# Optimization experiments

Measured on AMD Instinct MI355X. Metric: run time of the kernel, lower is better.

## Reference

```python
import jax, jax.numpy as jnp
import numpy as np

N_NODES = 50000
N_EDGES = 800000
D = 256


def gcn_conv(x, edge_index, W, b, n_nodes):
    """PyG-style GCNConv: add self-loops, symmetric norm, linear, scatter-add."""
    # add self loops
    loops = jnp.arange(n_nodes, dtype=edge_index.dtype)
    src = jnp.concatenate([edge_index[0], loops])  # message sources
    dst = jnp.concatenate([edge_index[1], loops])  # aggregation targets
    # symmetric normalization: deg computed on targets (incl. self loops)
    deg = jax.ops.segment_sum(jnp.ones_like(dst, dtype=x.dtype), dst,
                              num_segments=n_nodes)
    dinv = jnp.where(deg > 0, jax.lax.rsqrt(deg), 0.0)
    norm = dinv[src] * dinv[dst]  # [E+N]
    h = x @ W  # [N, out]
    msg = h[src] * norm[:, None]  # gather + scale, [E+N, out]
    out = jax.ops.segment_sum(msg, dst, num_segments=n_nodes)  # scatter-add
    return out + b


def setup_inputs() -> dict:
    key = jax.random.key(0)
    k1, k2, k3, k4 = jax.random.split(key, 4)
    x = jax.random.normal(k1, (N_NODES, D), dtype=jnp.float32)
    edge_index = jax.random.randint(k2, (2, N_EDGES), 0, N_NODES, dtype=jnp.int64)
    s = 1.0 / np.sqrt(D)
    W1 = jax.random.normal(k3, (D, D), dtype=jnp.float32) * s
    W2 = jax.random.normal(k4, (D, D), dtype=jnp.float32) * s
    b1 = jnp.zeros((D,), dtype=jnp.float32)
    b2 = jnp.zeros((D,), dtype=jnp.float32)
    return {"x": x, "edge_index": edge_index, "W1": W1, "b1": b1,
            "W2": W2, "b2": b2}


def reference(x, edge_index, W1, b1, W2, b2):
    n = x.shape[0]
    out = gcn_conv(x, edge_index, W1, b1, n)
    out = jax.nn.relu(out)  # dropout is identity in eval mode (p=0.2 in train)
    out = out + gcn_conv(x, edge_index, W2, b2, n)
    return out
```

## Files before the change

kernel.cpp:

```cpp
#include <hip/hip_runtime.h>
#include <hip/hip_bf16.h>

#define DIM 256
#define CAP 64
#define GEMM_BX 64

typedef short bf16x8 __attribute__((ext_vector_type(8)));
typedef float f32x4  __attribute__((ext_vector_type(4)));
typedef unsigned int u32x4 __attribute__((ext_vector_type(4)));

__device__ __forceinline__ unsigned short f2b(float f) {
    union { __hip_bfloat16 h; unsigned short u; } cv;
    cv.h = __float2bfloat16(f);
    return cv.u;
}
__device__ __forceinline__ float b2f(unsigned short u) {
    return __uint_as_float(((unsigned)u) << 16);
}
__device__ __forceinline__ void acc8(u32x4 u, float* a) {
    a[0] += __uint_as_float(u.x << 16); a[1] += __uint_as_float(u.x & 0xffff0000u);
    a[2] += __uint_as_float(u.y << 16); a[3] += __uint_as_float(u.y & 0xffff0000u);
    a[4] += __uint_as_float(u.z << 16); a[5] += __uint_as_float(u.z & 0xffff0000u);
    a[6] += __uint_as_float(u.w << 16); a[7] += __uint_as_float(u.w & 0xffff0000u);
}

#define OFF_FILL   0
#define OFF_WT1    262144
#define OFF_WT2    393216
#define OFF_BUCKET 524288
#define OFF_AGG    6924544ull
#define OFF_YB     32524544ull
#define NEED_BF    (OFF_YB + 25600000ull)

__global__ void k_fill(const int* __restrict__ src, const int* __restrict__ dst,
                       int* __restrict__ fill, unsigned short* __restrict__ bucket, int nE) {
    int e = blockIdx.x * blockDim.x + threadIdx.x;
    if (e < nE) {
        int d = dst[e];
        int pos = atomicAdd(&fill[d], 1);
        if (pos < CAP) bucket[d * CAP + pos] = (unsigned short)src[e];
    }
}

__global__ void k_prep(const float* __restrict__ x, const int* __restrict__ fill,
                       u32x4* __restrict__ yb,
                       const float* __restrict__ W1, const float* __restrict__ W2,
                       unsigned short* __restrict__ wt1, unsigned short* __restrict__ wt2,
                       int nybBlocks, int n8) {
    if ((int)blockIdx.x < nybBlocks) {
        int t = blockIdx.x * 256 + threadIdx.x;
        if (t < n8) {
            int node = t >> 5, g = t & 31;
            int nN = n8 >> 5;
            float d = rsqrtf((float)(1 + fill[node]));
            const f32x4* xp = (const f32x4*)x + t * 2;
            f32x4 v0 = xp[0], v1 = xp[1];
            u32x4 r;
            r.x = (unsigned)f2b(d * v0.x) | ((unsigned)f2b(d * v0.y) << 16);
            r.y = (unsigned)f2b(d * v0.z) | ((unsigned)f2b(d * v0.w) << 16);
            r.z = (unsigned)f2b(d * v1.x) | ((unsigned)f2b(d * v1.y) << 16);
            r.w = (unsigned)f2b(d * v1.z) | ((unsigned)f2b(d * v1.w) << 16);
            yb[((size_t)(g >> 2) * nN + node) * 4 + (g & 3)] = r;
        }
    } else {
        int t = (blockIdx.x - nybBlocks) * 256 + threadIdx.x;
        if (t < DIM * DIM) {
            int k = t & 255, nn = t >> 8;
            wt1[t] = f2b(W1[k * DIM + nn]);
            wt2[t] = f2b(W2[k * DIM + nn]);
        }
    }
}

__global__ void k_agg_bf(const u32x4* __restrict__ yb, const int* __restrict__ fill,
                         const unsigned short* __restrict__ bucket,
                         u32x4* __restrict__ aggbf, int n) {
    int slice = blockIdx.x & 7;
    int nb    = blockIdx.x >> 3;
    int tid   = threadIdx.x;
    int node  = nb * 64 + (tid >> 2);
    int ch    = tid & 3;
    if (node >= n) return;

    const u32x4* ybs = yb + (size_t)slice * n * 4;

    float a[8];
    u32x4 s = ybs[(size_t)node * 4 + ch];
#pragma unroll
    for (int i = 0; i < 8; i++) a[i] = 0.f;
    acc8(s, a);

    int c = __builtin_nontemporal_load(&fill[node]);
    float di = rsqrtf((float)(1 + c));
    if (c > CAP) c = CAP;
    const unsigned short* bk = bucket + (size_t)node * CAP;

    int kfull = c & ~7;
    for (int k = 0; k < kfull; k += 8) {
        u32x4 iv = __builtin_nontemporal_load((const u32x4*)(bk + k));
        int j0 = iv.x & 0xffff, j1 = iv.x >> 16;
        int j2 = iv.y & 0xffff, j3 = iv.y >> 16;
        int j4 = iv.z & 0xffff, j5 = iv.z >> 16;
        int j6 = iv.w & 0xffff, j7 = iv.w >> 16;
        u32x4 r0 = ybs[(size_t)j0 * 4 + ch];
        u32x4 r1 = ybs[(size_t)j1 * 4 + ch];
        u32x4 r2 = ybs[(size_t)j2 * 4 + ch];
        u32x4 r3 = ybs[(size_t)j3 * 4 + ch];
        u32x4 r4 = ybs[(size_t)j4 * 4 + ch];
        u32x4 r5 = ybs[(size_t)j5 * 4 + ch];
        u32x4 r6 = ybs[(size_t)j6 * 4 + ch];
        u32x4 r7 = ybs[(size_t)j7 * 4 + ch];
        acc8(r0, a); acc8(r1, a); acc8(r2, a); acc8(r3, a);
        acc8(r4, a); acc8(r5, a); acc8(r6, a); acc8(r7, a);
    }
    int rem = c - kfull;
    if (rem) {
        u32x4 iv = __builtin_nontemporal_load((const u32x4*)(bk + kfull));
        int j0 = iv.x & 0xffff, j1 = iv.x >> 16;
        int j2 = iv.y & 0xffff, j3 = iv.y >> 16;
        int j4 = iv.z & 0xffff, j5 = iv.z >> 16;
        int j6 = iv.w & 0xffff;
        j1 = (rem > 1) ? j1 : 0;
        j2 = (rem > 2) ? j2 : 0;
        j3 = (rem > 3) ? j3 : 0;
        j4 = (rem > 4) ? j4 : 0;
        j5 = (rem > 5) ? j5 : 0;
        j6 = (rem > 6) ? j6 : 0;
        u32x4 r0 = ybs[(size_t)j0 * 4 + ch];
        u32x4 r1 = ybs[(size_t)j1 * 4 + ch];
        u32x4 r2 = ybs[(size_t)j2 * 4 + ch];
        u32x4 r3 = ybs[(size_t)j3 * 4 + ch];
        u32x4 r4 = ybs[(size_t)j4 * 4 + ch];
        u32x4 r5 = ybs[(size_t)j5 * 4 + ch];
        u32x4 r6 = ybs[(size_t)j6 * 4 + ch];
        acc8(r0, a);
        if (rem > 1) acc8(r1, a);
        if (rem > 2) acc8(r2, a);
        if (rem > 3) acc8(r3, a);
        if (rem > 4) acc8(r4, a);
        if (rem > 5) acc8(r5, a);
        if (rem > 6) acc8(r6, a);
    }

    u32x4 r;
    r.x = (unsigned)f2b(a[0] * di) | ((unsigned)f2b(a[1] * di) << 16);
    r.y = (unsigned)f2b(a[2] * di) | ((unsigned)f2b(a[3] * di) << 16);
    r.z = (unsigned)f2b(a[4] * di) | ((unsigned)f2b(a[5] * di) << 16);
    r.w = (unsigned)f2b(a[6] * di) | ((unsigned)f2b(a[7] * di) << 16);
    __builtin_nontemporal_store(r, &aggbf[(size_t)node * 32 + slice * 4 + ch]);
}

__global__ void k_agg_f32(const float4* __restrict__ x4, const int* __restrict__ fill,
                          const unsigned short* __restrict__ bucket,
                          ushort4* __restrict__ aggbf, int n) {
    int node = (blockIdx.x * blockDim.x + threadIdx.x) >> 6;
    int lane = threadIdx.x & 63;
    if (node >= n) return;

    int c = fill[node];
    float di = rsqrtf((float)(1 + c));
    if (c > CAP) c = CAP;

    float4 xi = x4[(size_t)node * 64 + lane];
    float a0 = di * xi.x, a1 = di * xi.y, a2 = di * xi.z, a3 = di * xi.w;

    const unsigned short* bk = bucket + (size_t)node * CAP;
    for (int k = 0; k < c; k++) {
        int j = bk[k];
        float dj = rsqrtf((float)(1 + fill[j]));
        float4 xj = x4[(size_t)j * 64 + lane];
        a0 += dj * xj.x; a1 += dj * xj.y; a2 += dj * xj.z; a3 += dj * xj.w;
    }
    ushort4 r;
    r.x = f2b(a0 * di); r.y = f2b(a1 * di);
    r.z = f2b(a2 * di); r.w = f2b(a3 * di);
    aggbf[(size_t)node * 64 + lane] = r;
}

__launch_bounds__(256, 2)
__global__ void k_gemm(const short* __restrict__ aggbf,
                       const short* __restrict__ wt1, const short* __restrict__ wt2,
                       const float* __restrict__ b1, const float* __restrict__ b2,
                       float* __restrict__ out, int n, int ntiles) {
    __shared__ u32x4 bs[2048];

    int c0  = blockIdx.y * 32;
    int tid = threadIdx.x;

#pragma unroll
    for (int i = 0; i < 8; i++) {
        int l = tid + i * 256;
        int m = l >> 10, rem = l & 1023, nn = rem >> 5, p = rem & 31;
        const short* base = (m == 0) ? wt1 : wt2;
        const u32x4* sp = (const u32x4*)(base + (size_t)(c0 + nn) * DIM) + p;
        bs[(m << 10) + (nn << 5) + (p ^ nn)] = *sp;
    }
    __syncthreads();

    int lane = tid & 63;
    int wave = tid >> 6;
    int lrow = lane & 15;
    int quad = lane >> 4;

    bf16x8 w1r[2][8], w2r[2][8];
#pragma unroll
    for (int ct = 0; ct < 2; ct++) {
        int nn = ct * 16 + lrow;
#pragma unroll
        for (int s = 0; s < 8; s++) {
            int p = (4 * s + quad) ^ nn;
            u32x4 u = bs[(nn << 5) + p];
            u32x4 v = bs[1024 + (nn << 5) + p];
            __builtin_memcpy(&w1r[ct][s], &u, 16);
            __builtin_memcpy(&w2r[ct][s], &v, 16);
        }
    }

    f32x4 bb1[2], bb2[2];
#pragma unroll
    for (int ct = 0; ct < 2; ct++) {
        bb1[ct] = *(const f32x4*)&b1[c0 + ct * 16 + quad * 4];
        bb2[ct] = *(const f32x4*)&b2[c0 + ct * 16 + quad * 4];
    }

    for (int t = blockIdx.x; t < ntiles; t += gridDim.x) {
        int row = t * 64 + wave * 16 + lrow;
        int r = (row < n) ? row : 0;
        const short* ap = aggbf + (size_t)r * DIM + quad * 8;

        bf16x8 A[8];
#pragma unroll
        for (int s = 0; s < 8; s++) A[s] = *(const bf16x8*)(ap + s * 32);

        f32x4 acc1[2], acc2[2];
#pragma unroll
        for (int ct = 0; ct < 2; ct++) {
            acc1[ct] = (f32x4){0.f, 0.f, 0.f, 0.f};
            acc2[ct] = (f32x4){0.f, 0.f, 0.f, 0.f};
        }

#pragma unroll
        for (int s = 0; s < 8; s++) {
#pragma unroll
            for (int ct = 0; ct < 2; ct++) {
                acc1[ct] = __builtin_amdgcn_mfma_f32_16x16x32_bf16(w1r[ct][s], A[s], acc1[ct], 0, 0, 0);
                acc2[ct] = __builtin_amdgcn_mfma_f32_16x16x32_bf16(w2r[ct][s], A[s], acc2[ct], 0, 0, 0);
            }
        }

        if (row < n) {
#pragma unroll
            for (int ct = 0; ct < 2; ct++) {
                f32x4 v;
#pragma unroll
                for (int i = 0; i < 4; i++)
                    v[i] = fmaxf(acc1[ct][i] + bb1[ct][i], 0.f) + acc2[ct][i] + bb2[ct][i];
                f32x4* dstp = (f32x4*)&out[(size_t)row * DIM + c0 + ct * 16 + quad * 4];
                __builtin_nontemporal_store(v, dstp);
            }
        }
    }
}

extern "C" void kernel_launch(void* const* d_in, const int* in_sizes, int n_in,
                              void* d_out, int out_size, void* d_ws, size_t ws_size,
                              hipStream_t stream) {
    const float* x  = (const float*)d_in[0];
    const int*   ei = (const int*)d_in[1];
    const float* W1 = (const float*)d_in[2];
    const float* b1 = (const float*)d_in[3];
    const float* W2 = (const float*)d_in[4];
    const float* b2 = (const float*)d_in[5];
    float* out = (float*)d_out;

    int n = in_sizes[0] / DIM;
    int E = in_sizes[1] / 2;
    const int* src = ei;
    const int* dst = ei + E;

    char* ws = (char*)d_ws;
    int*            fill   = (int*)(ws + OFF_FILL);
    unsigned short* wt1    = (unsigned short*)(ws + OFF_WT1);
    unsigned short* wt2    = (unsigned short*)(ws + OFF_WT2);
    unsigned short* bucket = (unsigned short*)(ws + OFF_BUCKET);
    char*           aggp   = ws + OFF_AGG;
    u32x4*          yb     = (u32x4*)(ws + OFF_YB);

    (void)hipMemsetAsync(fill, 0, n * sizeof(int), stream);

    k_fill<<<(E + 255) / 256, 256, 0, stream>>>(src, dst, fill, bucket, E);

    bool use_bf = (ws_size >= NEED_BF);
    if (use_bf) {
        int n8 = n * (DIM / 8);
        int nybBlocks = (n8 + 255) / 256;
        k_prep<<<nybBlocks + 256, 256, 0, stream>>>(x, fill, yb, W1, W2, wt1, wt2,
                                                    nybBlocks, n8);
        int aggBlocks = ((n + 63) / 64) * 8;
        k_agg_bf<<<aggBlocks, 256, 0, stream>>>(yb, fill, bucket, (u32x4*)aggp, n);
    } else {
        k_prep<<<256, 256, 0, stream>>>(x, fill, yb, W1, W2, wt1, wt2, 0, 0);
        int aggBlocks = (n * 64 + 255) / 256;
        k_agg_f32<<<aggBlocks, 256, 0, stream>>>((const float4*)x, fill, bucket,
                                                 (ushort4*)aggp, n);
    }

    int ntiles = (n + 63) / 64;
    dim3 ggrid(GEMM_BX, DIM / 32);
    k_gemm<<<ggrid, 256, 0, stream>>>((const short*)aggp, (const short*)wt1,
                                      (const short*)wt2, b1, b2, out, n, ntiles);
}
```

Before: 257.6 us.

## Split each node's neighbor gather across 8 lanes and reduce with shuffles

The bf16 aggregation kernel now gives each node 32 lanes, 8 edge groups times 4 channels, instead of 4 lanes. Each lane gathers a strided subset of the node's neighbors, and the partial sums are combined with xor shuffles. The goal is to raise memory-level parallelism and remove the serial per-thread neighbor loop and its tail divergence, at the cost of 8x more threads, shuffle reductions and scalar index loads. The prep kernel is also reindexed so its writes to the sliced layout are contiguous, while its reads from x become strided.

```diff
diff --git a/kernel.cpp b/kernel.cpp
--- a/kernel.cpp
+++ b/kernel.cpp
@@ -13,9 +13,6 @@
     union { __hip_bfloat16 h; unsigned short u; } cv;
     cv.h = __float2bfloat16(f);
     return cv.u;
-}
-__device__ __forceinline__ float b2f(unsigned short u) {
-    return __uint_as_float(((unsigned)u) << 16);
 }
 __device__ __forceinline__ void acc8(u32x4 u, float* a) {
     a[0] += __uint_as_float(u.x << 16); a[1] += __uint_as_float(u.x & 0xffff0000u);
@@ -50,17 +47,21 @@
     if ((int)blockIdx.x < nybBlocks) {
         int t = blockIdx.x * 256 + threadIdx.x;
         if (t < n8) {
-            int node = t >> 5, g = t & 31;
-            int nN = n8 >> 5;
+            int nN   = n8 >> 5;
+            int s    = t / (nN * 4);
+            int rest = t - s * (nN * 4);
+            int node = rest >> 2;
+            int ch   = rest & 3;
+            int g    = s * 4 + ch;
             float d = rsqrtf((float)(1 + fill[node]));
-            const f32x4* xp = (const f32x4*)x + t * 2;
+            const f32x4* xp = (const f32x4*)x + ((size_t)node * 32 + g) * 2;
             f32x4 v0 = xp[0], v1 = xp[1];
             u32x4 r;
             r.x = (unsigned)f2b(d * v0.x) | ((unsigned)f2b(d * v0.y) << 16);
             r.y = (unsigned)f2b(d * v0.z) | ((unsigned)f2b(d * v0.w) << 16);
             r.z = (unsigned)f2b(d * v1.x) | ((unsigned)f2b(d * v1.y) << 16);
             r.w = (unsigned)f2b(d * v1.z) | ((unsigned)f2b(d * v1.w) << 16);
-            yb[((size_t)(g >> 2) * nN + node) * 4 + (g & 3)] = r;
+            yb[t] = r;
         }
     } else {
         int t = (blockIdx.x - nybBlocks) * 256 + threadIdx.x;
@@ -78,76 +79,56 @@
     int slice = blockIdx.x & 7;
     int nb    = blockIdx.x >> 3;
     int tid   = threadIdx.x;
-    int node  = nb * 64 + (tid >> 2);
-    int ch    = tid & 3;
-    if (node >= n) return;
+    int wv    = tid >> 6;
+    int lane  = tid & 63;
+    int nd    = lane >> 5;
+    int e     = (lane >> 2) & 7;
+    int ch    = lane & 3;
+    int node  = nb * 8 + wv * 2 + nd;
+    bool valid = node < n;
+    int nodeC = valid ? node : 0;
 
     const u32x4* ybs = yb + (size_t)slice * n * 4;
 
-    float a[8];
-    u32x4 s = ybs[(size_t)node * 4 + ch];
-#pragma unroll
-    for (int i = 0; i < 8; i++) a[i] = 0.f;
-    acc8(s, a);
-
-    int c = __builtin_nontemporal_load(&fill[node]);
+    int c = __builtin_nontemporal_load(&fill[nodeC]);
     float di = rsqrtf((float)(1 + c));
     if (c > CAP) c = CAP;
-    const unsigned short* bk = bucket + (size_t)node * CAP;
-
-    int kfull = c & ~7;
-    for (int k = 0; k < kfull; k += 8) {
-        u32x4 iv = __builtin_nontemporal_load((const u32x4*)(bk + k));
-        int j0 = iv.x & 0xffff, j1 = iv.x >> 16;
-        int j2 = iv.y & 0xffff, j3 = iv.y >> 16;
-        int j4 = iv.z & 0xffff, j5 = iv.z >> 16;
-        int j6 = iv.w & 0xffff, j7 = iv.w >> 16;
-        u32x4 r0 = ybs[(size_t)j0 * 4 + ch];
-        u32x4 r1 = ybs[(size_t)j1 * 4 + ch];
-        u32x4 r2 = ybs[(size_t)j2 * 4 + ch];
-        u32x4 r3 = ybs[(size_t)j3 * 4 + ch];
-        u32x4 r4 = ybs[(size_t)j4 * 4 + ch];
-        u32x4 r5 = ybs[(size_t)j5 * 4 + ch];
-        u32x4 r6 = ybs[(size_t)j6 * 4 + ch];
-        u32x4 r7 = ybs[(size_t)j7 * 4 + ch];
-        acc8(r0, a); acc8(r1, a); acc8(r2, a); acc8(r3, a);
-        acc8(r4, a); acc8(r5, a); acc8(r6, a); acc8(r7, a);
-    }
-    int rem = c - kfull;
-    if (rem) {
-        u32x4 iv = __builtin_nontemporal_load((const u32x4*)(bk + kfull));
-        int j0 = iv.x & 0xffff, j1 = iv.x >> 16;
-        int j2 = iv.y & 0xffff, j3 = iv.y >> 16;
-        int j4 = iv.z & 0xffff, j5 = iv.z >> 16;
-        int j6 = iv.w & 0xffff;
-        j1 = (rem > 1) ? j1 : 0;
-        j2 = (rem > 2) ? j2 : 0;
-        j3 = (rem > 3) ? j3 : 0;
-        j4 = (rem > 4) ? j4 : 0;
-        j5 = (rem > 5) ? j5 : 0;
-        j6 = (rem > 6) ? j6 : 0;
-        u32x4 r0 = ybs[(size_t)j0 * 4 + ch];
-        u32x4 r1 = ybs[(size_t)j1 * 4 + ch];
-        u32x4 r2 = ybs[(size_t)j2 * 4 + ch];
-        u32x4 r3 = ybs[(size_t)j3 * 4 + ch];
-        u32x4 r4 = ybs[(size_t)j4 * 4 + ch];
-        u32x4 r5 = ybs[(size_t)j5 * 4 + ch];
-        u32x4 r6 = ybs[(size_t)j6 * 4 + ch];
-        acc8(r0, a);
-        if (rem > 1) acc8(r1, a);
-        if (rem > 2) acc8(r2, a);
-        if (rem > 3) acc8(r3, a);
-        if (rem > 4) acc8(r4, a);
-        if (rem > 5) acc8(r5, a);
-        if (rem > 6) acc8(r6, a);
-    }
-
-    u32x4 r;
-    r.x = (unsigned)f2b(a[0] * di) | ((unsigned)f2b(a[1] * di) << 16);
-    r.y = (unsigned)f2b(a[2] * di) | ((unsigned)f2b(a[3] * di) << 16);
-    r.z = (unsigned)f2b(a[4] * di) | ((unsigned)f2b(a[5] * di) << 16);
-    r.w = (unsigned)f2b(a[6] * di) | ((unsigned)f2b(a[7] * di) << 16);
-    __builtin_nontemporal_store(r, &aggbf[(size_t)node * 32 + slice * 4 + ch]);
+    const unsigned short* bk = bucket + (size_t)nodeC * CAP;
+
+    unsigned short j0 = __builtin_nontemporal_load(bk + e);
+    unsigned short j1 = __builtin_nontemporal_load(bk + e + 8);
+    unsigned short j2 = __builtin_nontemporal_load(bk + e + 16);
+    unsigned short j3 = __builtin_nontemporal_load(bk + e + 24);
+
+    float a[8];
+#pragma unroll
+    for (int i = 0; i < 8; i++) a[i] = 0.f;
+
+    if (e == 0)      acc8(ybs[(size_t)nodeC * 4 + ch], a);
+    if (e < c)       acc8(ybs[(size_t)j0 * 4 + ch], a);
+    if (e + 8 < c)   acc8(ybs[(size_t)j1 * 4 + ch], a);
+    if (e + 16 < c)  acc8(ybs[(size_t)j2 * 4 + ch], a);
+    if (e + 24 < c)  acc8(ybs[(size_t)j3 * 4 + ch], a);
+    for (int k = 32 + e; k < c; k += 8) {
+        unsigned short jj = __builtin_nontemporal_load(bk + k);
+        acc8(ybs[(size_t)jj * 4 + ch], a);
+    }
+
+#pragma unroll
+    for (int i = 0; i < 8; i++) a[i] += __shfl_xor(a[i], 4, 64);
+#pragma unroll
+    for (int i = 0; i < 8; i++) a[i] += __shfl_xor(a[i], 8, 64);
+#pragma unroll
+    for (int i = 0; i < 8; i++) a[i] += __shfl_xor(a[i], 16, 64);
+
+    if (valid && e == 0) {
+        u32x4 r;
+        r.x = (unsigned)f2b(a[0] * di) | ((unsigned)f2b(a[1] * di) << 16);
+        r.y = (unsigned)f2b(a[2] * di) | ((unsigned)f2b(a[3] * di) << 16);
+        r.z = (unsigned)f2b(a[4] * di) | ((unsigned)f2b(a[5] * di) << 16);
+        r.w = (unsigned)f2b(a[6] * di) | ((unsigned)f2b(a[7] * di) << 16);
+        __builtin_nontemporal_store(r, &aggbf[(size_t)node * 32 + slice * 4 + ch]);
+    }
 }
 
 __global__ void k_agg_f32(const float4* __restrict__ x4, const int* __restrict__ fill,
@@ -296,7 +277,7 @@
         int nybBlocks = (n8 + 255) / 256;
         k_prep<<<nybBlocks + 256, 256, 0, stream>>>(x, fill, yb, W1, W2, wt1, wt2,
                                                     nybBlocks, n8);
-        int aggBlocks = ((n + 63) / 64) * 8;
+        int aggBlocks = ((n + 7) / 8) * 8;
         k_agg_bf<<<aggBlocks, 256, 0, stream>>>(yb, fill, bucket, (u32x4*)aggp, n);
     } else {
         k_prep<<<256, 256, 0, stream>>>(x, fill, yb, W1, W2, wt1, wt2, 0, 0);
```

Measured after the change: 276.5 us. 1.07x slower.
